# Optimization experiments

Measured on AMD Instinct MI355X. Metric: run time of the kernel, lower is better.

Reference implementation:

```python
import jax, jax.numpy as jnp
import numpy as np

B, C, H, W = 16, 512, 64, 64


def setup_inputs() -> dict:
    key = jax.random.key(0)
    ks = jax.random.split(key, 5)
    s = 0.02  # init scale for projection weights
    return {
        "x": jax.random.normal(ks[0], (B, C, H, W), jnp.float32),
        "Wqkv": jax.random.normal(ks[1], (3 * C, C), jnp.float32) * s,
        "bqkv": jnp.zeros((3 * C,), jnp.float32),
        "Wm": jax.random.normal(ks[2], (2 * C, C), jnp.float32) * s,
        "bm": jnp.zeros((2 * C,), jnp.float32),
        "Wg": jax.random.normal(ks[3], (C, 2 * C), jnp.float32) * s,
        "bg": jnp.zeros((C,), jnp.float32),
        "Wr": jax.random.normal(ks[4], (C, C), jnp.float32) * s,
        "br": jnp.zeros((C,), jnp.float32),
    }


def reference(x, Wqkv, bqkv, Wm, bm, Wg, bg, Wr, br):
    b, c, h, w = x.shape
    n = h * w
    xf = x.reshape(b, c, n)  # [B,C,N]
    # qkv projection: [B,3C,N] -> q,k,v each [B,C,N]
    qkv = jnp.einsum('oc,bcn->bon', Wqkv, xf) + bqkv[None, :, None]
    q, k, v = qkv[:, :c], qkv[:, c:2 * c], qkv[:, 2 * c:]
    # modulation from v: mq, mk each [B,C,N]
    mqk = jnp.einsum('oc,bcn->bon', Wm, v) + bm[None, :, None]
    mq, mk = mqk[:, :c], mqk[:, c:]
    _q = jax.nn.softmax(-jax.nn.relu(q * mq), axis=-1)   # softmax over N
    _k = jax.nn.relu(k * mk)                             # [B,C,N]
    # channel attention: [B,C,N] @ [B,N,C] -> [B,C,C]
    scores = jnp.einsum('bcn,bdn->bcd', _q, _k) / jnp.sqrt(jnp.float32(c))
    attn = jax.nn.softmax(scores, axis=-1)
    y = jnp.einsum('bcd,bdn->bcn', attn, v)              # [B,C,N]
    y2d = y.reshape(b, c, h, w)
    # gated residual: g = sigmoid(W_g @ cat(y, x))
    catf = jnp.concatenate([y, xf], axis=1)              # [B,2C,N]
    g = jax.nn.sigmoid(jnp.einsum('oc,bcn->bon', Wg, catf) + bg[None, :, None]).reshape(b, c, h, w)
    r = (jnp.einsum('oc,bcn->bon', Wr, xf) + br[None, :, None]).reshape(b, c, h, w)
    out = g * r + (1.0 - g) * y2d
    return (out, attn)
```

## Files before the change

kernel.cpp:

```cpp
#include <hip/hip_runtime.h>
#include <math.h>

#define Bb 16
#define Cc 512
#define Nn 4096
#define CN (512L * 4096)

typedef __bf16 bf16x8 __attribute__((ext_vector_type(8)));
typedef float  floatx4 __attribute__((ext_vector_type(4)));

__device__ __forceinline__ unsigned short f2bf(float f) {
    unsigned int u = __float_as_uint(f);
    unsigned int r = (u + 0x7FFFu + ((u >> 16) & 1u)) >> 16;
    return (unsigned short)r;
}
__device__ __forceinline__ float bf2f(unsigned short s) {
    return __uint_as_float(((unsigned int)s) << 16);
}

__device__ __forceinline__ void gload16(const void* g, void* l) {
    __builtin_amdgcn_global_load_lds(
        (const __attribute__((address_space(1))) unsigned int*)g,
        (__attribute__((address_space(3))) unsigned int*)l,
        16, 0, 0);
}

template<int OUTF32, int SPLIT>
__global__ __launch_bounds__(256) void gemm_bt(
    const unsigned short* __restrict__ A1,
    const unsigned short* __restrict__ A2, int lda, int asplit,
    const unsigned short* __restrict__ B, int ldb,
    const float* __restrict__ bias,
    void* __restrict__ Cv, int ldc,
    int K, float scale,
    long sA, long sB, long sC)
{
    __shared__ __align__(16) unsigned short Alds[8 * 512];
    __shared__ __align__(16) unsigned short Blds[8 * 512];

    const int t    = threadIdx.x;
    const int lane = t & 63;
    const int wave = t >> 6;
    const int m0 = blockIdx.y * 128;
    const int n0 = blockIdx.x * 128;
    const int wm = (wave >> 1) * 64;
    const int wn = (wave & 1) * 64;

    const unsigned short* Ab1 = A1 + (size_t)blockIdx.z * sA;
    const unsigned short* Ab2 = SPLIT ? (A2 + (size_t)blockIdx.z * sA) : nullptr;
    const unsigned short* Bb_ = B + (size_t)blockIdx.z * sB;

    const int srow = lane & 15;
    const int sk   = (lane >> 4) * 8;

    floatx4 acc[4][4] = {};

    for (int k0 = 0; k0 < K; k0 += 32) {
        const unsigned short* Asrc;
        int kk;
        if (SPLIT && k0 >= asplit) { Asrc = Ab2; kk = k0 - asplit; }
        else                       { Asrc = Ab1; kk = k0; }
#pragma unroll
        for (int s = 0; s < 2; ++s) {
            int sub = wave * 2 + s;
            const unsigned short* ga = Asrc + (size_t)(m0 + sub * 16 + srow) * lda + kk + sk;
            const unsigned short* gb = Bb_  + (size_t)(n0 + sub * 16 + srow) * ldb + k0 + sk;
            gload16(ga, &Alds[sub * 512]);
            gload16(gb, &Blds[sub * 512]);
        }
        __syncthreads();

        bf16x8 af[4], bfr[4];
#pragma unroll
        for (int i = 0; i < 4; ++i) {
            af[i]  = *(const bf16x8*)&Alds[((wm >> 4) + i) * 512 + lane * 8];
            bfr[i] = *(const bf16x8*)&Blds[((wn >> 4) + i) * 512 + lane * 8];
        }
#pragma unroll
        for (int i = 0; i < 4; ++i)
#pragma unroll
            for (int j = 0; j < 4; ++j)
                acc[i][j] = __builtin_amdgcn_mfma_f32_16x16x32_bf16(af[i], bfr[j], acc[i][j], 0, 0, 0);
        __syncthreads();
    }

    const int rbase = (lane >> 4) * 4;
    const int cofs  = lane & 15;
#pragma unroll
    for (int j = 0; j < 4; ++j) {
        int col = n0 + wn + j * 16 + cofs;
        float bv = bias ? bias[col] : 0.0f;
#pragma unroll
        for (int i = 0; i < 4; ++i) {
#pragma unroll
            for (int r = 0; r < 4; ++r) {
                int row = m0 + wm + i * 16 + rbase + r;
                float v = acc[i][j][r] * scale + bv;
                if (OUTF32) {
                    float* C = (float*)Cv + (size_t)blockIdx.z * sC;
                    C[(size_t)row * ldc + col] = v;
                } else {
                    unsigned short* C = (unsigned short*)Cv + (size_t)blockIdx.z * sC;
                    C[(size_t)row * ldc + col] = f2bf(v);
                }
            }
        }
    }
}

__global__ __launch_bounds__(256) void wcast(const float* __restrict__ w,
                                             unsigned short* __restrict__ o, int n)
{
    int i = (blockIdx.x * 256 + threadIdx.x) * 4;
    float4 v = *(const float4*)&w[i];
    ushort4 u;
    u.x = f2bf(v.x); u.y = f2bf(v.y); u.z = f2bf(v.z); u.w = f2bf(v.w);
    *(ushort4*)&o[i] = u;
}

__global__ __launch_bounds__(256) void transpose_x(const float* __restrict__ x,
                                                   unsigned short* __restrict__ xp)
{
    __shared__ unsigned short tile[64][65];
    const float* X = x + (size_t)blockIdx.z * CN;
    unsigned short* O = xp + (size_t)blockIdx.z * CN;
    int n0 = blockIdx.x * 64, c0 = blockIdx.y * 64;
    int tq = (threadIdx.x & 15) * 4, tr = threadIdx.x >> 4;
#pragma unroll
    for (int r = 0; r < 4; ++r) {
        int cl = tr + r * 16;
        float4 v = *(const float4*)&X[(size_t)(c0 + cl) * 4096 + n0 + tq];
        tile[tq + 0][cl] = f2bf(v.x);
        tile[tq + 1][cl] = f2bf(v.y);
        tile[tq + 2][cl] = f2bf(v.z);
        tile[tq + 3][cl] = f2bf(v.w);
    }
    __syncthreads();
#pragma unroll
    for (int r = 0; r < 4; ++r) {
        int nl = tr + r * 16;
        ushort4 o;
        o.x = tile[nl][tq + 0]; o.y = tile[nl][tq + 1];
        o.z = tile[nl][tq + 2]; o.w = tile[nl][tq + 3];
        *(ushort4*)&O[(size_t)(n0 + nl) * 512 + c0 + tq] = o;
    }
}

__global__ __launch_bounds__(256) void qk_transform(
    const unsigned short* __restrict__ qkv, const unsigned short* __restrict__ mqk,
    unsigned short* __restrict__ T, int coff, int neg)
{
    __shared__ __align__(8) unsigned short tile[64][68];
    const unsigned short* S1 = qkv + (size_t)blockIdx.z * (4096L * 1536) + coff;
    const unsigned short* S2 = mqk + (size_t)blockIdx.z * (4096L * 1024) + coff;
    unsigned short* O = T + (size_t)blockIdx.z * CN;
    int n0 = blockIdx.x * 64, c0 = blockIdx.y * 64;
    int tq = (threadIdx.x & 15) * 4, tr = threadIdx.x >> 4;
#pragma unroll
    for (int r = 0; r < 4; ++r) {
        int nl = tr + r * 16;
        ushort4 a = *(const ushort4*)&S1[(size_t)(n0 + nl) * 1536 + c0 + tq];
        ushort4 m = *(const ushort4*)&S2[(size_t)(n0 + nl) * 1024 + c0 + tq];
        float f0 = fmaxf(bf2f(a.x) * bf2f(m.x), 0.0f);
        float f1 = fmaxf(bf2f(a.y) * bf2f(m.y), 0.0f);
        float f2 = fmaxf(bf2f(a.z) * bf2f(m.z), 0.0f);
        float f3 = fmaxf(bf2f(a.w) * bf2f(m.w), 0.0f);
        if (neg) { f0 = -f0; f1 = -f1; f2 = -f2; f3 = -f3; }
        ushort4 p;
        p.x = f2bf(f0); p.y = f2bf(f1); p.z = f2bf(f2); p.w = f2bf(f3);
        *(ushort4*)&tile[nl][tq] = p;
    }
    __syncthreads();
#pragma unroll
    for (int r = 0; r < 4; ++r) {
        int cl = tr + r * 16;
        ushort4 o;
        o.x = tile[tq + 0][cl]; o.y = tile[tq + 1][cl];
        o.z = tile[tq + 2][cl]; o.w = tile[tq + 3][cl];
        *(ushort4*)&O[(size_t)(c0 + cl) * 4096 + n0 + tq] = o;
    }
}

__global__ __launch_bounds__(256) void qsoftmax_bf(unsigned short* __restrict__ Q)
{
    unsigned short* p = Q + (size_t)blockIdx.x * 4096;
    const int t = threadIdx.x;
    const int lane = t & 63;
    const int wv = t >> 6;
    __shared__ float red[8];

    float vals[16];
    float mx = -1e30f;
#pragma unroll
    for (int i = 0; i < 16; ++i) {
        float v = bf2f(p[t + i * 256]);
        vals[i] = v;
        mx = fmaxf(mx, v);
    }
#pragma unroll
    for (int off = 32; off > 0; off >>= 1) mx = fmaxf(mx, __shfl_xor(mx, off));
    if (lane == 0) red[wv] = mx;
    __syncthreads();
    mx = fmaxf(fmaxf(red[0], red[1]), fmaxf(red[2], red[3]));

    float sum = 0.0f;
#pragma unroll
    for (int i = 0; i < 16; ++i) {
        vals[i] = __expf(vals[i] - mx);
        sum += vals[i];
    }
#pragma unroll
    for (int off = 32; off > 0; off >>= 1) sum += __shfl_xor(sum, off);
    if (lane == 0) red[4 + wv] = sum;
    __syncthreads();
    sum = red[4] + red[5] + red[6] + red[7];
    float inv = 1.0f / sum;
#pragma unroll
    for (int i = 0; i < 16; ++i) p[t + i * 256] = f2bf(vals[i] * inv);
}

__global__ __launch_bounds__(256) void attn_softmax_dual(
    float* __restrict__ attnf, unsigned short* __restrict__ attnb)
{
    float* p = attnf + (size_t)blockIdx.x * 512;
    unsigned short* pb = attnb + (size_t)blockIdx.x * 512;
    const int t = threadIdx.x;
    const int lane = t & 63;
    const int wv = t >> 6;
    __shared__ float red[8];

    float v0 = p[t], v1 = p[t + 256];
    float mx = fmaxf(v0, v1);
#pragma unroll
    for (int off = 32; off > 0; off >>= 1) mx = fmaxf(mx, __shfl_xor(mx, off));
    if (lane == 0) red[wv] = mx;
    __syncthreads();
    mx = fmaxf(fmaxf(red[0], red[1]), fmaxf(red[2], red[3]));

    float e0 = __expf(v0 - mx);
    float e1 = __expf(v1 - mx);
    float sum = e0 + e1;
#pragma unroll
    for (int off = 32; off > 0; off >>= 1) sum += __shfl_xor(sum, off);
    if (lane == 0) red[4 + wv] = sum;
    __syncthreads();
    sum = red[4] + red[5] + red[6] + red[7];
    float inv = 1.0f / sum;
    float a0 = e0 * inv, a1 = e1 * inv;
    p[t] = a0;        p[t + 256] = a1;
    pb[t] = f2bf(a0); pb[t + 256] = f2bf(a1);
}

__global__ __launch_bounds__(256) void final_fuse(
    const unsigned short* __restrict__ gl, const unsigned short* __restrict__ rr,
    const unsigned short* __restrict__ yy, float* __restrict__ out)
{
    __shared__ __align__(16) float tile[64][68];
    size_t bo = (size_t)blockIdx.z * CN;
    const unsigned short* G_ = gl + bo;
    const unsigned short* R_ = rr + bo;
    const unsigned short* Y_ = yy + bo;
    float* O = out + bo;
    int n0 = blockIdx.x * 64, c0 = blockIdx.y * 64;
    int tq = (threadIdx.x & 15) * 4, tr = threadIdx.x >> 4;
#pragma unroll
    for (int r = 0; r < 4; ++r) {
        int nl = tr + r * 16;
        size_t base = (size_t)(n0 + nl) * 512 + c0 + tq;
        ushort4 g4 = *(const ushort4*)&G_[base];
        ushort4 r4 = *(const ushort4*)&R_[base];
        ushort4 y4 = *(const ushort4*)&Y_[base];
        float4 o;
        float g;
        g = 1.0f / (1.0f + __expf(-bf2f(g4.x))); o.x = g * bf2f(r4.x) + (1.0f - g) * bf2f(y4.x);
        g = 1.0f / (1.0f + __expf(-bf2f(g4.y))); o.y = g * bf2f(r4.y) + (1.0f - g) * bf2f(y4.y);
        g = 1.0f / (1.0f + __expf(-bf2f(g4.z))); o.z = g * bf2f(r4.z) + (1.0f - g) * bf2f(y4.z);
        g = 1.0f / (1.0f + __expf(-bf2f(g4.w))); o.w = g * bf2f(r4.w) + (1.0f - g) * bf2f(y4.w);
        *(float4*)&tile[nl][tq] = o;
    }
    __syncthreads();
#pragma unroll
    for (int r = 0; r < 4; ++r) {
        int cl = tr + r * 16;
        float4 o;
        o.x = tile[tq + 0][cl]; o.y = tile[tq + 1][cl];
        o.z = tile[tq + 2][cl]; o.w = tile[tq + 3][cl];
        *(float4*)&O[(size_t)(c0 + cl) * 4096 + n0 + tq] = o;
    }
}

extern "C" void kernel_launch(void* const* d_in, const int* in_sizes, int n_in,
                              void* d_out, int out_size, void* d_ws, size_t ws_size,
                              hipStream_t stream)
{
    const float* x    = (const float*)d_in[0];
    const float* Wqkv = (const float*)d_in[1];
    const float* bqkv = (const float*)d_in[2];
    const float* Wm   = (const float*)d_in[3];
    const float* bm   = (const float*)d_in[4];
    const float* Wg   = (const float*)d_in[5];
    const float* bg   = (const float*)d_in[6];
    const float* Wr   = (const float*)d_in[7];
    const float* br   = (const float*)d_in[8];

    float* out      = (float*)d_out;
    float* attn_all = out + (size_t)Bb * CN;

    unsigned short* wq_bf = (unsigned short*)d_ws;
    unsigned short* wm_bf = wq_bf + 1536 * 512;
    unsigned short* wg_bf = wm_bf + 1024 * 512;
    unsigned short* wr_bf = wg_bf + 512 * 1024;
    unsigned short* dyn   = wr_bf + 512 * 512;
    const size_t fixed_bytes = (size_t)(1536 * 512 + 1024 * 512 + 512 * 1024 + 512 * 512) * 2;
    const size_t per_batch_bytes = (size_t)4096 * 4096 * 2;

    int G = 16;
    while (G > 1 && fixed_bytes + (size_t)G * per_batch_bytes > ws_size) G >>= 1;

    dim3 blk(256);
    const float inv_sqrt_c = 0.044194173824159216f;

    wcast<<<1536 * 512 / 1024, blk, 0, stream>>>(Wqkv, wq_bf, 1536 * 512);
    wcast<<<1024 * 512 / 1024, blk, 0, stream>>>(Wm,   wm_bf, 1024 * 512);
    wcast<<<512 * 1024 / 1024, blk, 0, stream>>>(Wg,   wg_bf, 512 * 1024);
    wcast<<<512 * 512  / 1024, blk, 0, stream>>>(Wr,   wr_bf, 512 * 512);

    for (int b0 = 0; b0 < Bb; b0 += G) {
        unsigned short* xp   = dyn;
        unsigned short* qkvp = xp   + (size_t)G * 4096 * 512;
        unsigned short* mqkp = qkvp + (size_t)G * 4096 * 1536;
        unsigned short* qp   = mqkp + (size_t)G * 4096 * 1024;
        unsigned short* kp   = qp   + (size_t)G * CN;
        unsigned short* yp   = mqkp;
        unsigned short* glp  = mqkp + (size_t)G * CN;
        unsigned short* rp   = qp;
        unsigned short* abf  = kp;

        const float* xg   = x + (size_t)b0 * CN;
        float* outg       = out + (size_t)b0 * CN;
        float* attng      = attn_all + (size_t)b0 * 512 * 512;

        transpose_x<<<dim3(64, 8, G), blk, 0, stream>>>(xg, xp);

        gemm_bt<0, 0><<<dim3(12, 32, G), blk, 0, stream>>>(
            xp, nullptr, 512, 0, wq_bf, 512, bqkv, qkvp, 1536,
            512, 1.0f, 4096L * 512, 0L, 4096L * 1536);

        gemm_bt<0, 0><<<dim3(8, 32, G), blk, 0, stream>>>(
            qkvp + 1024, nullptr, 1536, 0, wm_bf, 512, bm, mqkp, 1024,
            512, 1.0f, 4096L * 1536, 0L, 4096L * 1024);

        qk_transform<<<dim3(64, 8, G), blk, 0, stream>>>(qkvp, mqkp, qp, 0, 1);
        qk_transform<<<dim3(64, 8, G), blk, 0, stream>>>(qkvp, mqkp, kp, 512, 0);

        qsoftmax_bf<<<G * 512, blk, 0, stream>>>(qp);

        gemm_bt<1, 0><<<dim3(4, 4, G), blk, 0, stream>>>(
            qp, nullptr, 4096, 0, kp, 4096, nullptr, attng, 512,
            4096, inv_sqrt_c, CN, CN, 512L * 512);

        attn_softmax_dual<<<G * 512, blk, 0, stream>>>(attng, abf);

        gemm_bt<0, 0><<<dim3(4, 32, G), blk, 0, stream>>>(
            qkvp + 1024, nullptr, 1536, 0, abf, 512, nullptr, yp, 512,
            512, 1.0f, 4096L * 1536, 512L * 512, 4096L * 512);

        gemm_bt<0, 1><<<dim3(4, 32, G), blk, 0, stream>>>(
            yp, xp, 512, 512, wg_bf, 1024, bg, glp, 512,
            1024, 1.0f, 4096L * 512, 0L, 4096L * 512);

        gemm_bt<0, 0><<<dim3(4, 32, G), blk, 0, stream>>>(
            xp, nullptr, 512, 0, wr_bf, 512, br, rp, 512,
            512, 1.0f, 4096L * 512, 0L, 4096L * 512);

        final_fuse<<<dim3(64, 8, G), blk, 0, stream>>>(glp, rp, yp, outg);
    }
}
```

Measured before the change: 1.269 ms.

## Double-buffer LDS tiles in bf16 GEMM to overlap global loads with MFMA

Converts the GEMM main loop to a two-stage LDS ping-pong: the next K-tile is fetched with global_load_lds while MFMAs run on the current one, gated by explicit vmcnt waits and raw barriers. It also precomputes the global pointers and raises wave priority around the MFMA block. This targets exposed global-load latency in the synchronous load-then-compute loop, at the cost of doubled LDS use and reliance on hand-written waitcnt ordering.

```diff
diff --git a/kernel.cpp b/kernel.cpp
--- a/kernel.cpp
+++ b/kernel.cpp
@@ -35,8 +35,8 @@
     int K, float scale,
     long sA, long sB, long sC)
 {
-    __shared__ __align__(16) unsigned short Alds[8 * 512];
-    __shared__ __align__(16) unsigned short Blds[8 * 512];
+    __shared__ __align__(16) unsigned short Alds[2][8 * 512];
+    __shared__ __align__(16) unsigned short Blds[2][8 * 512];
 
     const int t    = threadIdx.x;
     const int lane = t & 63;
@@ -52,36 +52,58 @@
 
     const int srow = lane & 15;
     const int sk   = (lane >> 4) * 8;
+    const int sub0 = wave * 2;
+
+    const unsigned short* gA0 = Ab1 + (size_t)(m0 + (sub0    ) * 16 + srow) * lda + sk;
+    const unsigned short* gA1 = Ab1 + (size_t)(m0 + (sub0 + 1) * 16 + srow) * lda + sk;
+    const unsigned short* gB0 = Bb_ + (size_t)(n0 + (sub0    ) * 16 + srow) * ldb + sk;
+    const unsigned short* gB1 = Bb_ + (size_t)(n0 + (sub0 + 1) * 16 + srow) * ldb + sk;
+    const ptrdiff_t sjump = SPLIT ? (Ab2 - Ab1) - (ptrdiff_t)asplit : 0;
+
+    auto stage = [&](int buf, int k0) {
+        const unsigned short* a0 = gA0 + k0;
+        const unsigned short* a1 = gA1 + k0;
+        if (SPLIT && k0 >= asplit) { a0 += sjump; a1 += sjump; }
+        gload16(a0,       &Alds[buf][(sub0    ) * 512]);
+        gload16(gB0 + k0, &Blds[buf][(sub0    ) * 512]);
+        gload16(a1,       &Alds[buf][(sub0 + 1) * 512]);
+        gload16(gB1 + k0, &Blds[buf][(sub0 + 1) * 512]);
+    };
 
     floatx4 acc[4][4] = {};
 
-    for (int k0 = 0; k0 < K; k0 += 32) {
-        const unsigned short* Asrc;
-        int kk;
-        if (SPLIT && k0 >= asplit) { Asrc = Ab2; kk = k0 - asplit; }
-        else                       { Asrc = Ab1; kk = k0; }
-#pragma unroll
-        for (int s = 0; s < 2; ++s) {
-            int sub = wave * 2 + s;
-            const unsigned short* ga = Asrc + (size_t)(m0 + sub * 16 + srow) * lda + kk + sk;
-            const unsigned short* gb = Bb_  + (size_t)(n0 + sub * 16 + srow) * ldb + k0 + sk;
-            gload16(ga, &Alds[sub * 512]);
-            gload16(gb, &Blds[sub * 512]);
+    const int nt = K >> 5;
+    int cur = 0;
+    stage(0, 0);
+
+    for (int ti = 0; ti < nt; ++ti) {
+        if (ti + 1 < nt) {
+            stage(cur ^ 1, (ti + 1) << 5);
+            asm volatile("s_waitcnt vmcnt(4)" ::: "memory");
+        } else {
+            asm volatile("s_waitcnt vmcnt(0)" ::: "memory");
         }
-        __syncthreads();
+        __builtin_amdgcn_s_barrier();
+        __builtin_amdgcn_sched_barrier(0);
 
         bf16x8 af[4], bfr[4];
 #pragma unroll
         for (int i = 0; i < 4; ++i) {
-            af[i]  = *(const bf16x8*)&Alds[((wm >> 4) + i) * 512 + lane * 8];
-            bfr[i] = *(const bf16x8*)&Blds[((wn >> 4) + i) * 512 + lane * 8];
+            af[i]  = *(const bf16x8*)&Alds[cur][((wm >> 4) + i) * 512 + lane * 8];
+            bfr[i] = *(const bf16x8*)&Blds[cur][((wn >> 4) + i) * 512 + lane * 8];
         }
+        __builtin_amdgcn_s_setprio(1);
 #pragma unroll
         for (int i = 0; i < 4; ++i)
 #pragma unroll
             for (int j = 0; j < 4; ++j)
                 acc[i][j] = __builtin_amdgcn_mfma_f32_16x16x32_bf16(af[i], bfr[j], acc[i][j], 0, 0, 0);
-        __syncthreads();
+        __builtin_amdgcn_s_setprio(0);
+
+        asm volatile("s_waitcnt lgkmcnt(0)" ::: "memory");
+        __builtin_amdgcn_s_barrier();
+        __builtin_amdgcn_sched_barrier(0);
+        cur ^= 1;
     }
 
     const int rbase = (lane >> 4) * 4;
```

After: 1.246 ms. Within noise of the previous version (-1.8%).
